# Performance work log

Hardware: AMD Instinct MI355X
Metric: run time of the kernel (lower is better)

Reference implementation:

```python
import jax, jax.numpy as jnp
import numpy as np

WIN = 7
NUM_HEADS = 12
DIM = 384
HEAD_DIM = DIM // NUM_HEADS
SEQ = WIN * WIN


def _relative_position_index():
    ch, cw = np.meshgrid(np.arange(WIN), np.arange(WIN), indexing='ij')
    coords = np.stack([ch, cw]).reshape(2, -1)            # [2, 49]
    rel = coords[:, :, None] - coords[:, None, :]          # [2, 49, 49]
    rel = rel.transpose(1, 2, 0)
    rel[:, :, 0] += WIN - 1
    rel[:, :, 1] += WIN - 1
    rel[:, :, 0] *= 2 * WIN - 1
    return rel.sum(-1).astype(np.int32)                    # [49, 49]


def setup_inputs() -> dict:
    key = jax.random.key(0)
    ks = jax.random.split(key, 12)
    bz = 2048
    mw = 64  # windows per image
    s = 0.02
    inp = {
        'hidden_states': jax.random.normal(ks[0], (bz, SEQ, DIM), jnp.float32),
        'attention_mask': jax.random.normal(ks[1], (mw, SEQ, SEQ), jnp.float32),
        'qW': jax.random.normal(ks[2], (DIM, DIM), jnp.float32) * s,
        'qb': jnp.zeros((DIM,), jnp.float32),
        'kW': jax.random.normal(ks[3], (DIM, DIM), jnp.float32) * s,
        'kb': jnp.zeros((DIM,), jnp.float32),
        'vW': jax.random.normal(ks[4], (DIM, DIM), jnp.float32) * s,
        'vb': jnp.zeros((DIM,), jnp.float32),
        'oW': jax.random.normal(ks[5], (DIM, DIM), jnp.float32) * s,
        'ob': jnp.zeros((DIM,), jnp.float32),
        'bias_table': jax.random.normal(ks[6], ((2 * WIN - 1) ** 2, NUM_HEADS), jnp.float32) * s,
        'rel_idx': jnp.asarray(_relative_position_index()),
    }
    return inp


def reference(hidden_states, attention_mask, qW, qb, kW, kb, vW, vb, oW, ob, bias_table, rel_idx):
    bz, seq, dim = hidden_states.shape
    H, D = NUM_HEADS, HEAD_DIM

    def heads(x, W, b):
        y = jnp.einsum('bsd,de->bse', hidden_states, W) + b
        return y.reshape(bz, seq, H, D).transpose(0, 2, 1, 3)  # [b, h, s, d]

    q = heads(hidden_states, qW, qb)
    k = heads(hidden_states, kW, kb)
    v = heads(hidden_states, vW, vb)

    scores = jnp.einsum('bhsd,bhtd->bhst', q, k) / jnp.sqrt(jnp.float32(D))

    # relative position bias: gather [49*49, H] -> [H, 49, 49]
    rpb = bias_table[rel_idx.reshape(-1)].reshape(seq, seq, H).transpose(2, 0, 1)
    scores = scores + rpb[None]

    mw = attention_mask.shape[0]
    scores = scores.reshape(bz // mw, mw, H, seq, seq) + attention_mask[None, :, None]
    scores = scores.reshape(bz, H, seq, seq)

    attn = jax.nn.softmax(scores, axis=-1)
    ctx = jnp.einsum('bhst,bhtd->bhsd', attn, v)
    ctx = ctx.transpose(0, 2, 1, 3).reshape(bz, seq, dim)
    return jnp.einsum('bsd,de->bse', ctx, oW) + ob
```

## Files before the change

kernel.cpp:

```cpp
#include <hip/hip_runtime.h>


typedef unsigned short u16;
typedef unsigned int   u32;
typedef short bf16x8 __attribute__((ext_vector_type(8)));
typedef float f32x4  __attribute__((ext_vector_type(4)));
typedef u16   u16x8  __attribute__((ext_vector_type(8)));
typedef u16   u16x4  __attribute__((ext_vector_type(4)));

#define NWIN   2048
#define SEQ    49
#define DIM    384
#define NH     12
#define HD     32
#define MTOT   (NWIN*SEQ)
#define WELEM  (DIM*DIM)

__device__ __forceinline__ u16 f2b(float f) {
    union { float f; unsigned u; } c; c.f = f;
    unsigned u = c.u;
    u += 0x7FFFu + ((u >> 16) & 1u);
    return (u16)(u >> 16);
}

__global__ __launch_bounds__(256) void prep_x(const float* __restrict__ X, u16* __restrict__ Xb) {
    int i = blockIdx.x * 256 + threadIdx.x;
    float4 v = ((const float4*)X)[i];
    u16x4 o; o[0]=f2b(v.x); o[1]=f2b(v.y); o[2]=f2b(v.z); o[3]=f2b(v.w);
    ((u16x4*)Xb)[i] = o;
}

__global__ __launch_bounds__(256) void prep_w(const float* __restrict__ qW, const float* __restrict__ kW,
                                              const float* __restrict__ vW, const float* __restrict__ oW,
                                              u16* __restrict__ Wt) {
    int t = blockIdx.x * 256 + threadIdx.x;
    int m = t / WELEM; int rem = t - m * WELEM;
    int k = rem / DIM; int n = rem - k * DIM;
    const float* src = (m==0) ? qW : (m==1) ? kW : (m==2) ? vW : oW;
    Wt[m*WELEM + n*DIM + k] = f2b(src[rem]);
}

__global__ __launch_bounds__(256) void prep_comb(const float* __restrict__ bt, const int* __restrict__ ridx,
                                                 const float* __restrict__ mask, float* __restrict__ comb) {
    int idx = blockIdx.x * 256 + threadIdx.x;
    int t = idx & 63, s = (idx >> 6) & 63;
    int hw = idx >> 12;
    int h = hw % NH, wm = hw / NH;
    float v = -1e30f;
    if (s < SEQ && t < SEQ) {
        int st = s * SEQ + t;
        v = bt[ridx[st] * NH + h] + mask[wm * (SEQ*SEQ) + st];
    }
    comb[idx] = v;
}

__device__ __forceinline__ void gload_lds16(const void* g, void* l) {
    __builtin_amdgcn_global_load_lds((const __attribute__((address_space(1))) void*)g,
                                     (__attribute__((address_space(3))) void*)l, 16, 0, 0);
}

__device__ __forceinline__ void stage_tile_async(const u16* __restrict__ g0, u16* lds, int wv, int lane) {
    const int r8   = lane >> 3;
    const int scol = ((lane & 7) * 8) ^ (r8 << 3);
    const u16* src = g0 + (wv * 8 + r8) * DIM + scol;
    u16*       dst = lds + wv * 512 + lane * 8;
    #pragma unroll
    for (int i = 0; i < 4; i++)
        gload_lds16(src + i * 32 * DIM, dst + i * 2048);
}

__device__ __forceinline__ void gemm_tile(const u16* __restrict__ Abase, const u16* __restrict__ Bbase,
                                          f32x4 (&acc)[4][4]) {
    __shared__ __align__(16) u16 As[128 * 64];
    __shared__ __align__(16) u16 Bs[128 * 64];
    const int tid = threadIdx.x, wave = tid >> 6, lane = tid & 63;
    const int wm = wave >> 1, wn = wave & 1;
    const int swzl = (lane & 7) << 3;
    for (int kt = 0; kt < 6; kt++) {
        __syncthreads();
        stage_tile_async(Abase + kt * 64, As, wave, lane);
        stage_tile_async(Bbase + kt * 64, Bs, wave, lane);
        __syncthreads();
        #pragma unroll
        for (int kk = 0; kk < 2; kk++) {
            const int co = (kk * 32 + (lane >> 4) * 8) ^ swzl;
            bf16x8 a[4], b[4];
            #pragma unroll
            for (int mi = 0; mi < 4; mi++)
                a[mi] = *(const bf16x8*)&As[(wm * 64 + mi * 16 + (lane & 15)) * 64 + co];
            #pragma unroll
            for (int ni = 0; ni < 4; ni++)
                b[ni] = *(const bf16x8*)&Bs[(wn * 64 + ni * 16 + (lane & 15)) * 64 + co];
            #pragma unroll
            for (int mi = 0; mi < 4; mi++)
                #pragma unroll
                for (int ni = 0; ni < 4; ni++)
                    acc[mi][ni] = __builtin_amdgcn_mfma_f32_16x16x32_bf16(a[mi], b[ni], acc[mi][ni], 0, 0, 0);
        }
    }
}

__global__ __launch_bounds__(256) void qkv_gemm(const u16* __restrict__ Xb, const u16* __restrict__ Wt,
                                                const float* __restrict__ qb, const float* __restrict__ kb,
                                                const float* __restrict__ vb,
                                                u16* __restrict__ Qo, u16* __restrict__ Ko, u16* __restrict__ Vo) {
    const int bid = blockIdx.x;
    const int swz = (bid & 7) * 882 + (bid >> 3);
    const int mTile = swz / 9, p = swz - mTile * 9;
    const int mBase = mTile * 128;
    const int proj = p / 3, nBase = (p - proj * 3) * 128;
    f32x4 acc[4][4];
    #pragma unroll
    for (int mi = 0; mi < 4; mi++)
        #pragma unroll
        for (int ni = 0; ni < 4; ni++) { f32x4 z = {0.f,0.f,0.f,0.f}; acc[mi][ni] = z; }

    gemm_tile(Xb + mBase * DIM, Wt + proj * WELEM + nBase * DIM, acc);

    const float* bias = (proj==0) ? qb : (proj==1) ? kb : vb;
    u16* Out          = (proj==0) ? Qo : (proj==1) ? Ko : Vo;
    const float scale = (proj==0) ? 0.17677669529663687f : 1.0f;
    const int tid = threadIdx.x, wave = tid >> 6, lane = tid & 63;
    const int wm = wave >> 1, wn = wave & 1;

    float bias4[4]; int hh[4], dd[4];
    #pragma unroll
    for (int ni = 0; ni < 4; ni++) {
        int nin = nBase + wn * 64 + ni * 16 + (lane & 15);
        bias4[ni] = bias[nin]; hh[ni] = nin >> 5; dd[ni] = nin & 31;
    }
    #pragma unroll
    for (int mi = 0; mi < 4; mi++) {
        #pragma unroll
        for (int j = 0; j < 4; j++) {
            int gm = mBase + wm * 64 + mi * 16 + ((lane >> 4) << 2) + j;
            int bw = gm / SEQ, s = gm - bw * SEQ;
            int rowbase = (bw * (NH*SEQ) + s) * HD;
            #pragma unroll
            for (int ni = 0; ni < 4; ni++) {
                float val = (acc[mi][ni][j] + bias4[ni]) * scale;
                Out[rowbase + hh[ni] * (SEQ*HD) + dd[ni]] = f2b(val);
            }
        }
    }
}

__global__ __launch_bounds__(256) void attn_mfma(const u16* __restrict__ Qb, const u16* __restrict__ Kb,
                                                 const u16* __restrict__ Vb, const float* __restrict__ comb,
                                                 u16* __restrict__ Ctx) {
    const int tid = threadIdx.x, wv = tid >> 6, lane = tid & 63;
    const int r16 = lane & 15, g = lane >> 4;
    const int idx = blockIdx.x * 4 + wv;
    const int w = idx / NH, h = idx - w * NH;
    const int wm = w & 63;

    __shared__ __align__(16) u16 vlds[4][64 * HD];

    const u16* Qp = Qb + idx * (SEQ*HD);
    const u16* Kp = Kb + idx * (SEQ*HD);
    const u16* Vp = Vb + idx * (SEQ*HD);

    {
        u16x8 z8 = {0,0,0,0,0,0,0,0};
        #pragma unroll
        for (int c4 = 0; c4 < 4; c4++) {
            int c = c4 * 64 + lane;
            u16x8 val = z8;
            if ((c >> 2) < SEQ) val = *(const u16x8*)&Vp[c * 8];
            *(u16x8*)&vlds[wv][c * 8] = val;
        }
    }

    bf16x8 kf[4], qf[4];
    #pragma unroll
    for (int ti = 0; ti < 4; ti++) kf[ti] = *(const bf16x8*)&Kp[(ti*16 + r16)*HD + g*8];
    #pragma unroll
    for (int si = 0; si < 4; si++) qf[si] = *(const bf16x8*)&Qp[(si*16 + r16)*HD + g*8];

    f32x4 st[4][4];
    __builtin_amdgcn_s_setprio(1);
    #pragma unroll
    for (int ti = 0; ti < 4; ti++)
        #pragma unroll
        for (int si = 0; si < 4; si++) {
            f32x4 z = {0.f,0.f,0.f,0.f};
            st[ti][si] = __builtin_amdgcn_mfma_f32_16x16x32_bf16(kf[ti], qf[si], z, 0, 0, 0);
        }
    __builtin_amdgcn_s_setprio(0);

    const float* cp = comb + (size_t)(wm * NH + h) * 4096;
    #pragma unroll
    for (int ti = 0; ti < 4; ti++)
        #pragma unroll
        for (int si = 0; si < 4; si++) {
            const float4 c = *(const float4*)&cp[(si*16 + r16) * 64 + ti*16 + g*4];
            st[ti][si][0] += c.x; st[ti][si][1] += c.y; st[ti][si][2] += c.z; st[ti][si][3] += c.w;
        }

    #pragma unroll
    for (int si = 0; si < 4; si++) {
        float m = st[0][si][0];
        #pragma unroll
        for (int ti = 0; ti < 4; ti++)
            #pragma unroll
            for (int r = 0; r < 4; r++) m = fmaxf(m, st[ti][si][r]);
        m = fmaxf(m, __shfl_xor(m, 16));
        m = fmaxf(m, __shfl_xor(m, 32));
        float sum = 0.f;
        #pragma unroll
        for (int ti = 0; ti < 4; ti++)
            #pragma unroll
            for (int r = 0; r < 4; r++) {
                float p = __expf(st[ti][si][r] - m);
                st[ti][si][r] = p; sum += p;
            }
        sum += __shfl_xor(sum, 16);
        sum += __shfl_xor(sum, 32);
        float rs = 1.0f / sum;
        #pragma unroll
        for (int ti = 0; ti < 4; ti++)
            #pragma unroll
            for (int r = 0; r < 4; r++) st[ti][si][r] *= rs;
    }

    u32 pk[4][4][2];
    #pragma unroll
    for (int ti = 0; ti < 4; ti++)
        #pragma unroll
        for (int si = 0; si < 4; si++)
            #pragma unroll
            for (int q = 0; q < 2; q++) {
                u32 r;
                asm("v_cvt_pk_bf16_f32 %0, %1, %2" : "=v"(r) : "v"(st[ti][si][2*q]), "v"(st[ti][si][2*q+1]));
                pk[ti][si][q] = r;
            }

    bf16x8 pa[2][4];
    const int base_src = r16 + ((g & 1) << 5);
    #pragma unroll
    for (int kc = 0; kc < 2; kc++)
        #pragma unroll
        for (int si = 0; si < 4; si++) {
            union { u32 u[4]; bf16x8 v; } cv;
            #pragma unroll
            for (int jj = 0; jj < 4; jj++) {
                int srcl = base_src + ((jj >> 1) << 4);
                u32 x0 = (u32)__shfl((int)pk[kc*2 + 0][si][jj & 1], srcl);
                u32 x1 = (u32)__shfl((int)pk[kc*2 + 1][si][jj & 1], srcl);
                cv.u[jj] = (lane >= 32) ? x1 : x0;
            }
            pa[kc][si] = cv.v;
        }

    bf16x8 vf[2][2];
    #pragma unroll
    for (int kc = 0; kc < 2; kc++)
        #pragma unroll
        for (int nt = 0; nt < 2; nt++) {
            bf16x8 v;
            #pragma unroll
            for (int i = 0; i < 8; i++)
                v[i] = (short)vlds[wv][(kc*32 + g*8 + i)*HD + nt*16 + r16];
            vf[kc][nt] = v;
        }

    f32x4 ct[4][2];
    __builtin_amdgcn_s_setprio(1);
    #pragma unroll
    for (int si = 0; si < 4; si++)
        #pragma unroll
        for (int nt = 0; nt < 2; nt++) {
            f32x4 z = {0.f,0.f,0.f,0.f};
            z = __builtin_amdgcn_mfma_f32_16x16x32_bf16(pa[0][si], vf[0][nt], z, 0, 0, 0);
            ct[si][nt] = __builtin_amdgcn_mfma_f32_16x16x32_bf16(pa[1][si], vf[1][nt], z, 0, 0, 0);
        }
    __builtin_amdgcn_s_setprio(0);

    #pragma unroll
    for (int si = 0; si < 4; si++)
        #pragma unroll
        for (int r = 0; r < 4; r++) {
            int s = si*16 + g*4 + r;
            if (s < SEQ) {
                #pragma unroll
                for (int nt = 0; nt < 2; nt++)
                    Ctx[(w*SEQ + s)*DIM + h*HD + nt*16 + r16] = f2b(ct[si][nt][r]);
            }
        }
}

__global__ __launch_bounds__(256) void oproj_gemm(const u16* __restrict__ Cb, const u16* __restrict__ Wo,
                                                  const float* __restrict__ ob, float* __restrict__ out) {
    const int bid = blockIdx.x;
    const int swz = (bid & 7) * 294 + (bid >> 3);
    const int mTile = swz / 3, nTile = swz - mTile * 3;
    const int mBase = mTile * 128, nBase = nTile * 128;
    f32x4 acc[4][4];
    #pragma unroll
    for (int mi = 0; mi < 4; mi++)
        #pragma unroll
        for (int ni = 0; ni < 4; ni++) { f32x4 z = {0.f,0.f,0.f,0.f}; acc[mi][ni] = z; }

    gemm_tile(Cb + mBase * DIM, Wo + nBase * DIM, acc);

    const int tid = threadIdx.x, wave = tid >> 6, lane = tid & 63;
    const int wm = wave >> 1, wn = wave & 1;
    float ob4[4]; int gn4[4];
    #pragma unroll
    for (int ni = 0; ni < 4; ni++) {
        gn4[ni] = nBase + wn * 64 + ni * 16 + (lane & 15);
        ob4[ni] = ob[gn4[ni]];
    }
    #pragma unroll
    for (int mi = 0; mi < 4; mi++) {
        #pragma unroll
        for (int j = 0; j < 4; j++) {
            int gm = mBase + wm * 64 + mi * 16 + ((lane >> 4) << 2) + j;
            #pragma unroll
            for (int ni = 0; ni < 4; ni++)
                out[gm * DIM + gn4[ni]] = acc[mi][ni][j] + ob4[ni];
        }
    }
}

extern "C" void kernel_launch(void* const* d_in, const int* in_sizes, int n_in,
                              void* d_out, int out_size, void* d_ws, size_t ws_size,
                              hipStream_t stream) {
    const float* hs   = (const float*)d_in[0];
    const float* mask = (const float*)d_in[1];
    const float* qW   = (const float*)d_in[2];
    const float* qb   = (const float*)d_in[3];
    const float* kW   = (const float*)d_in[4];
    const float* kb   = (const float*)d_in[5];
    const float* vW   = (const float*)d_in[6];
    const float* vb   = (const float*)d_in[7];
    const float* oW   = (const float*)d_in[8];
    const float* ob   = (const float*)d_in[9];
    const float* bt   = (const float*)d_in[10];
    const int*   ridx = (const int*)d_in[11];
    float* out = (float*)d_out;

    char* ws = (char*)d_ws;
    u16* Xb   = (u16*)(ws);
    u16* Ctx  = (u16*)(ws);
    u16* Qb   = (u16*)(ws + 77070336);
    u16* Kb   = (u16*)(ws + 154140672);
    u16* Vb   = (u16*)(ws + 231211008);
    u16* Wt   = (u16*)(ws + 308281344);
    float* comb = (float*)(ws + 309460992);

    prep_x   <<<37632, 256, 0, stream>>>(hs, Xb);
    prep_w   <<<2304, 256, 0, stream>>>(qW, kW, vW, oW, Wt);
    prep_comb<<<12288, 256, 0, stream>>>(bt, ridx, mask, comb);
    qkv_gemm <<<7056, 256, 0, stream>>>(Xb, Wt, qb, kb, vb, Qb, Kb, Vb);
    attn_mfma<<<6144, 256, 0, stream>>>(Qb, Kb, Vb, comb, Ctx);
    oproj_gemm<<<2352, 256, 0, stream>>>(Ctx, Wt + 3 * WELEM, ob, out);
}
```

Measured before the change: 378.1 us.

## Reuse bias/mask tile in LDS across windows sharing mask index

Regroups attention blocks so each block owns one (mask window, head) pair and loops its waves over 16 windows that share it. The combined bias+mask tile is loaded once into shared memory instead of being read from global memory per window-head. V is now read directly from global memory with scalar strided loads rather than staged in LDS, dropping the zero padding of rows past 49. This relies on masked probabilities being zero, and the gathers may be uncoalesced.

```diff
diff --git a/kernel.cpp b/kernel.cpp
--- a/kernel.cpp
+++ b/kernel.cpp
@@ -150,143 +150,146 @@
                                                  u16* __restrict__ Ctx) {
     const int tid = threadIdx.x, wv = tid >> 6, lane = tid & 63;
     const int r16 = lane & 15, g = lane >> 4;
-    const int idx = blockIdx.x * 4 + wv;
-    const int w = idx / NH, h = idx - w * NH;
-    const int wm = w & 63;
-
-    __shared__ __align__(16) u16 vlds[4][64 * HD];
-
-    const u16* Qp = Qb + idx * (SEQ*HD);
-    const u16* Kp = Kb + idx * (SEQ*HD);
-    const u16* Vp = Vb + idx * (SEQ*HD);
-
+    const int bid = blockIdx.x;
+    const int half = bid & 1, wh = bid >> 1;
+    const int wm = wh / NH, h = wh - wm * NH;
+
+    __shared__ float clds[64][68];
     {
-        u16x8 z8 = {0,0,0,0,0,0,0,0};
-        #pragma unroll
-        for (int c4 = 0; c4 < 4; c4++) {
-            int c = c4 * 64 + lane;
-            u16x8 val = z8;
-            if ((c >> 2) < SEQ) val = *(const u16x8*)&Vp[c * 8];
-            *(u16x8*)&vlds[wv][c * 8] = val;
-        }
-    }
-
-    bf16x8 kf[4], qf[4];
-    #pragma unroll
-    for (int ti = 0; ti < 4; ti++) kf[ti] = *(const bf16x8*)&Kp[(ti*16 + r16)*HD + g*8];
-    #pragma unroll
-    for (int si = 0; si < 4; si++) qf[si] = *(const bf16x8*)&Qp[(si*16 + r16)*HD + g*8];
-
-    f32x4 st[4][4];
-    __builtin_amdgcn_s_setprio(1);
-    #pragma unroll
-    for (int ti = 0; ti < 4; ti++)
+        const float4* cp = (const float4*)(comb + (size_t)wh * 4096);
+        #pragma unroll
+        for (int i0 = 0; i0 < 4; i0++) {
+            int i = i0 * 256 + tid;
+            float4 v = cp[i];
+            *(float4*)&clds[i >> 4][(i & 15) * 4] = v;
+        }
+    }
+    __syncthreads();
+
+    for (int it = 0; it < 4; it++) {
+        const int j = half * 16 + it * 4 + wv;
+        const int w = j * 64 + wm;
+        const int idx = w * NH + h;
+        const u16* Qp = Qb + idx * (SEQ*HD);
+        const u16* Kp = Kb + idx * (SEQ*HD);
+        const u16* Vp = Vb + idx * (SEQ*HD);
+
+        bf16x8 kf[4], qf[4];
+        #pragma unroll
+        for (int ti = 0; ti < 4; ti++) kf[ti] = *(const bf16x8*)&Kp[(ti*16 + r16)*HD + g*8];
+        #pragma unroll
+        for (int si = 0; si < 4; si++) qf[si] = *(const bf16x8*)&Qp[(si*16 + r16)*HD + g*8];
+
+        f32x4 st[4][4];
+        __builtin_amdgcn_s_setprio(1);
+        #pragma unroll
+        for (int ti = 0; ti < 4; ti++)
+            #pragma unroll
+            for (int si = 0; si < 4; si++) {
+                f32x4 z = {0.f,0.f,0.f,0.f};
+                st[ti][si] = __builtin_amdgcn_mfma_f32_16x16x32_bf16(kf[ti], qf[si], z, 0, 0, 0);
+            }
+        __builtin_amdgcn_s_setprio(0);
+
+        #pragma unroll
+        for (int ti = 0; ti < 4; ti++)
+            #pragma unroll
+            for (int si = 0; si < 4; si++) {
+                const float4 c = *(const float4*)&clds[si*16 + r16][ti*16 + g*4];
+                st[ti][si][0] += c.x; st[ti][si][1] += c.y; st[ti][si][2] += c.z; st[ti][si][3] += c.w;
+            }
+
         #pragma unroll
         for (int si = 0; si < 4; si++) {
-            f32x4 z = {0.f,0.f,0.f,0.f};
-            st[ti][si] = __builtin_amdgcn_mfma_f32_16x16x32_bf16(kf[ti], qf[si], z, 0, 0, 0);
-        }
-    __builtin_amdgcn_s_setprio(0);
-
-    const float* cp = comb + (size_t)(wm * NH + h) * 4096;
-    #pragma unroll
-    for (int ti = 0; ti < 4; ti++)
-        #pragma unroll
-        for (int si = 0; si < 4; si++) {
-            const float4 c = *(const float4*)&cp[(si*16 + r16) * 64 + ti*16 + g*4];
-            st[ti][si][0] += c.x; st[ti][si][1] += c.y; st[ti][si][2] += c.z; st[ti][si][3] += c.w;
-        }
-
-    #pragma unroll
-    for (int si = 0; si < 4; si++) {
-        float m = st[0][si][0];
+            float m = st[0][si][0];
+            #pragma unroll
+            for (int ti = 0; ti < 4; ti++)
+                #pragma unroll
+                for (int r = 0; r < 4; r++) m = fmaxf(m, st[ti][si][r]);
+            m = fmaxf(m, __shfl_xor(m, 16));
+            m = fmaxf(m, __shfl_xor(m, 32));
+            float sum = 0.f;
+            #pragma unroll
+            for (int ti = 0; ti < 4; ti++)
+                #pragma unroll
+                for (int r = 0; r < 4; r++) {
+                    float p = __expf(st[ti][si][r] - m);
+                    st[ti][si][r] = p; sum += p;
+                }
+            sum += __shfl_xor(sum, 16);
+            sum += __shfl_xor(sum, 32);
+            float rs = 1.0f / sum;
+            #pragma unroll
+            for (int ti = 0; ti < 4; ti++)
+                #pragma unroll
+                for (int r = 0; r < 4; r++) st[ti][si][r] *= rs;
+        }
+
+        u32 pk[4][4][2];
         #pragma unroll
         for (int ti = 0; ti < 4; ti++)
             #pragma unroll
-            for (int r = 0; r < 4; r++) m = fmaxf(m, st[ti][si][r]);
-        m = fmaxf(m, __shfl_xor(m, 16));
-        m = fmaxf(m, __shfl_xor(m, 32));
-        float sum = 0.f;
-        #pragma unroll
-        for (int ti = 0; ti < 4; ti++)
+            for (int si = 0; si < 4; si++)
+                #pragma unroll
+                for (int q = 0; q < 2; q++) {
+                    u32 r;
+                    asm("v_cvt_pk_bf16_f32 %0, %1, %2" : "=v"(r) : "v"(st[ti][si][2*q]), "v"(st[ti][si][2*q+1]));
+                    pk[ti][si][q] = r;
+                }
+
+        bf16x8 pa[2][4];
+        const int base_src = r16 + ((g & 1) << 5);
+        #pragma unroll
+        for (int kc = 0; kc < 2; kc++)
+            #pragma unroll
+            for (int si = 0; si < 4; si++) {
+                union { u32 u[4]; bf16x8 v; } cv;
+                #pragma unroll
+                for (int jj = 0; jj < 4; jj++) {
+                    int srcl = base_src + ((jj >> 1) << 4);
+                    u32 x0 = (u32)__shfl((int)pk[kc*2 + 0][si][jj & 1], srcl);
+                    u32 x1 = (u32)__shfl((int)pk[kc*2 + 1][si][jj & 1], srcl);
+                    cv.u[jj] = (lane >= 32) ? x1 : x0;
+                }
+                pa[kc][si] = cv.v;
+            }
+
+        bf16x8 vf[2][2];
+        #pragma unroll
+        for (int kc = 0; kc < 2; kc++)
+            #pragma unroll
+            for (int nt = 0; nt < 2; nt++) {
+                bf16x8 v;
+                #pragma unroll
+                for (int i = 0; i < 8; i++)
+                    v[i] = (short)Vp[(kc*32 + g*8 + i)*HD + nt*16 + r16];
+                vf[kc][nt] = v;
+            }
+
+        f32x4 ct[4][2];
+        __builtin_amdgcn_s_setprio(1);
+        #pragma unroll
+        for (int si = 0; si < 4; si++)
+            #pragma unroll
+            for (int nt = 0; nt < 2; nt++) {
+                f32x4 z = {0.f,0.f,0.f,0.f};
+                z = __builtin_amdgcn_mfma_f32_16x16x32_bf16(pa[0][si], vf[0][nt], z, 0, 0, 0);
+                ct[si][nt] = __builtin_amdgcn_mfma_f32_16x16x32_bf16(pa[1][si], vf[1][nt], z, 0, 0, 0);
+            }
+        __builtin_amdgcn_s_setprio(0);
+
+        #pragma unroll
+        for (int si = 0; si < 4; si++)
             #pragma unroll
             for (int r = 0; r < 4; r++) {
-                float p = __expf(st[ti][si][r] - m);
-                st[ti][si][r] = p; sum += p;
-            }
-        sum += __shfl_xor(sum, 16);
-        sum += __shfl_xor(sum, 32);
-        float rs = 1.0f / sum;
-        #pragma unroll
-        for (int ti = 0; ti < 4; ti++)
-            #pragma unroll
-            for (int r = 0; r < 4; r++) st[ti][si][r] *= rs;
-    }
-
-    u32 pk[4][4][2];
-    #pragma unroll
-    for (int ti = 0; ti < 4; ti++)
-        #pragma unroll
-        for (int si = 0; si < 4; si++)
-            #pragma unroll
-            for (int q = 0; q < 2; q++) {
-                u32 r;
-                asm("v_cvt_pk_bf16_f32 %0, %1, %2" : "=v"(r) : "v"(st[ti][si][2*q]), "v"(st[ti][si][2*q+1]));
-                pk[ti][si][q] = r;
-            }
-
-    bf16x8 pa[2][4];
-    const int base_src = r16 + ((g & 1) << 5);
-    #pragma unroll
-    for (int kc = 0; kc < 2; kc++)
-        #pragma unroll
-        for (int si = 0; si < 4; si++) {
-            union { u32 u[4]; bf16x8 v; } cv;
-            #pragma unroll
-            for (int jj = 0; jj < 4; jj++) {
-                int srcl = base_src + ((jj >> 1) << 4);
-                u32 x0 = (u32)__shfl((int)pk[kc*2 + 0][si][jj & 1], srcl);
-                u32 x1 = (u32)__shfl((int)pk[kc*2 + 1][si][jj & 1], srcl);
-                cv.u[jj] = (lane >= 32) ? x1 : x0;
-            }
-            pa[kc][si] = cv.v;
-        }
-
-    bf16x8 vf[2][2];
-    #pragma unroll
-    for (int kc = 0; kc < 2; kc++)
-        #pragma unroll
-        for (int nt = 0; nt < 2; nt++) {
-            bf16x8 v;
-            #pragma unroll
-            for (int i = 0; i < 8; i++)
-                v[i] = (short)vlds[wv][(kc*32 + g*8 + i)*HD + nt*16 + r16];
-            vf[kc][nt] = v;
-        }
-
-    f32x4 ct[4][2];
-    __builtin_amdgcn_s_setprio(1);
-    #pragma unroll
-    for (int si = 0; si < 4; si++)
-        #pragma unroll
-        for (int nt = 0; nt < 2; nt++) {
-            f32x4 z = {0.f,0.f,0.f,0.f};
-            z = __builtin_amdgcn_mfma_f32_16x16x32_bf16(pa[0][si], vf[0][nt], z, 0, 0, 0);
-            ct[si][nt] = __builtin_amdgcn_mfma_f32_16x16x32_bf16(pa[1][si], vf[1][nt], z, 0, 0, 0);
-        }
-    __builtin_amdgcn_s_setprio(0);
-
-    #pragma unroll
-    for (int si = 0; si < 4; si++)
-        #pragma unroll
-        for (int r = 0; r < 4; r++) {
-            int s = si*16 + g*4 + r;
-            if (s < SEQ) {
-                #pragma unroll
-                for (int nt = 0; nt < 2; nt++)
-                    Ctx[(w*SEQ + s)*DIM + h*HD + nt*16 + r16] = f2b(ct[si][nt][r]);
-            }
-        }
+                int s = si*16 + g*4 + r;
+                if (s < SEQ) {
+                    #pragma unroll
+                    for (int nt = 0; nt < 2; nt++)
+                        Ctx[(w*SEQ + s)*DIM + h*HD + nt*16 + r16] = f2b(ct[si][nt][r]);
+                }
+            }
+    }
 }
 
 __global__ __launch_bounds__(256) void oproj_gemm(const u16* __restrict__ Cb, const u16* __restrict__ Wo,
@@ -353,6 +356,6 @@
     prep_w   <<<2304, 256, 0, stream>>>(qW, kW, vW, oW, Wt);
     prep_comb<<<12288, 256, 0, stream>>>(bt, ridx, mask, comb);
     qkv_gemm <<<7056, 256, 0, stream>>>(Xb, Wt, qb, kb, vb, Qb, Kb, Vb);
-    attn_mfma<<<6144, 256, 0, stream>>>(Qb, Kb, Vb, comb, Ctx);
+    attn_mfma<<<1536, 256, 0, stream>>>(Qb, Kb, Vb, comb, Ctx);
     oproj_gemm<<<2352, 256, 0, stream>>>(Ctx, Wt + 3 * WELEM, ob, out);
 }
```

Measured after the change: 354.7 us. 6.2% less time.
